# Performance work log

Hardware: AMD Instinct MI355X
Metric: run time of the kernel (lower is better)

## Reference

```python
import jax, jax.numpy as jnp
import numpy as np

N = 100000   # nodes
E = 1200000  # edges
B = 64       # graphs
IN_DIM, HID, OUT_DIM = 128, 64, 2
N_HIDDEN = 2  # num_layers - 1 hidden GCN layers
EPS = 1e-5


def setup_inputs() -> dict:
    key = jax.random.key(0)
    ks = jax.random.split(key, 12)
    x = jax.random.normal(ks[0], (N, IN_DIM), dtype=jnp.float32)
    edge_index = jax.random.randint(ks[1], (2, E), 0, N, dtype=jnp.int64)
    batch = jnp.sort(jax.random.randint(ks[2], (N,), 0, B, dtype=jnp.int64))
    # Glorot-ish init for GCN linear weights (stored as [in, out])
    W_in = jax.random.normal(ks[3], (IN_DIM, HID), dtype=jnp.float32) / np.sqrt(IN_DIM)
    b_in = jnp.zeros((HID,), dtype=jnp.float32)
    W_h = jax.random.normal(ks[4], (N_HIDDEN, HID, HID), dtype=jnp.float32) / np.sqrt(HID)
    b_h = jnp.zeros((N_HIDDEN, HID), dtype=jnp.float32)
    W_out = jax.random.normal(ks[5], (HID, OUT_DIM), dtype=jnp.float32) / np.sqrt(HID)
    b_out = jnp.zeros((OUT_DIM,), dtype=jnp.float32)
    bn_gamma = jnp.ones((3, HID), dtype=jnp.float32)   # num_layers batch norms
    bn_beta = jnp.zeros((3, HID), dtype=jnp.float32)
    return {"x": x, "W_in": W_in, "b_in": b_in, "W_h": W_h, "b_h": b_h,
            "W_out": W_out, "b_out": b_out, "bn_gamma": bn_gamma,
            "bn_beta": bn_beta, "edge_index": edge_index, "batch": batch}


def _gcn_conv(h, W, b, src, dst, dinv):
    # PyG GCNConv: h' = D^-1/2 (A + I) D^-1/2 (h W) + b
    h = h @ W
    norm = dinv[src] * dinv[dst]                       # [E]
    agg = jax.ops.segment_sum(h[src] * norm[:, None], dst, num_segments=N)
    agg = agg + h * (dinv * dinv)[:, None]             # self-loop term
    return agg + b


def _batchnorm(h, gamma, beta):
    m = h.mean(axis=0)
    v = h.var(axis=0)  # biased, matches torch BN normalization
    return (h - m) * jax.lax.rsqrt(v + EPS) * gamma + beta


def reference(x, W_in, b_in, W_h, b_h, W_out, b_out, bn_gamma, bn_beta, edge_index, batch):
    src, dst = edge_index[0], edge_index[1]
    # degree with self-loops (edge weight 1)
    deg = jax.ops.segment_sum(jnp.ones((E,), x.dtype), dst, num_segments=N) + 1.0
    dinv = deg ** -0.5

    h = jax.nn.relu(_gcn_conv(x, W_in, b_in, src, dst, dinv))
    h = _batchnorm(h, bn_gamma[0], bn_beta[0])
    for i in range(N_HIDDEN):
        res = h
        h = jax.nn.relu(_gcn_conv(h, W_h[i], b_h[i], src, dst, dinv))
        h = _batchnorm(h, bn_gamma[i + 1], bn_beta[i + 1])
        h = h + res  # shapes match (HID == HID)
    h = _gcn_conv(h, W_out, b_out, src, dst, dinv)

    # global mean pool over batch segments
    sums = jax.ops.segment_sum(h, batch, num_segments=B)
    cnt = jax.ops.segment_sum(jnp.ones((N,), h.dtype), batch, num_segments=B)
    return sums / jnp.maximum(cnt, 1.0)[:, None]
```

## Files before the change

### kernel.cpp

```cpp
#include <hip/hip_runtime.h>
#include <hip/hip_fp16.h>


#define NN 100000
#define NE 1200000
#define NBATCH 64
#define IND 128
#define HID 64
#define EPSF 1e-5f
#define NBUCK 782
#define NPB 128
#define BCAP 2048

__global__ void k_escatter(const int* __restrict__ src, const int* __restrict__ dst,
                           int* __restrict__ bcur, unsigned long long* __restrict__ ebuf) {
  __shared__ int lh[NBUCK];
  __shared__ int lbase[NBUCK];
  int tid = threadIdx.x;
  for (int i = tid; i < NBUCK; i += 256) lh[i] = 0;
  __syncthreads();
  int base4 = blockIdx.x * 1024;
  int sv[16], dv[16], rk[16];
#pragma unroll
  for (int j = 0; j < 4; j++) {
    int i4 = base4 + j * 256 + tid;
    if (i4 * 4 < NE) {
      int4 s4 = ((const int4*)src)[i4];
      int4 d4 = ((const int4*)dst)[i4];
      sv[4 * j + 0] = s4.x; dv[4 * j + 0] = d4.x;
      sv[4 * j + 1] = s4.y; dv[4 * j + 1] = d4.y;
      sv[4 * j + 2] = s4.z; dv[4 * j + 2] = d4.z;
      sv[4 * j + 3] = s4.w; dv[4 * j + 3] = d4.w;
      rk[4 * j + 0] = atomicAdd(&lh[d4.x >> 7], 1);
      rk[4 * j + 1] = atomicAdd(&lh[d4.y >> 7], 1);
      rk[4 * j + 2] = atomicAdd(&lh[d4.z >> 7], 1);
      rk[4 * j + 3] = atomicAdd(&lh[d4.w >> 7], 1);
    } else {
      dv[4 * j + 0] = -1; dv[4 * j + 1] = -1;
      dv[4 * j + 2] = -1; dv[4 * j + 3] = -1;
    }
  }
  __syncthreads();
  for (int i = tid; i < NBUCK; i += 256) {
    int v = lh[i];
    lbase[i] = v ? atomicAdd(&bcur[i], v) : 0;
  }
  __syncthreads();
#pragma unroll
  for (int j = 0; j < 16; j++) {
    if (dv[j] >= 0) {
      int b = dv[j] >> 7;
      ebuf[(size_t)b * BCAP + lbase[b] + rk[j]] =
          (unsigned long long)(unsigned)sv[j] | ((unsigned long long)(unsigned)dv[j] << 32);
    }
  }
}

__global__ void k_bucket_csr(const unsigned long long* __restrict__ ebuf,
                             const int* __restrict__ bcur, int2* __restrict__ rc,
                             int* __restrict__ col) {
  __shared__ int ldeg[NPB];
  __shared__ int lcur[NPB];
  __shared__ int sred[NPB];
  int b = blockIdx.x, tid = threadIdx.x;
  int nbase = b * NPB;
  int e0 = b * BCAP;
  int cnt = bcur[b];
  if (tid < NPB) ldeg[tid] = 0;
  __syncthreads();
  for (int e = tid; e < cnt; e += 256) {
    int d = (int)(ebuf[e0 + e] >> 32) - nbase;
    atomicAdd(&ldeg[d], 1);
  }
  __syncthreads();
  if (tid < NPB) sred[tid] = ldeg[tid];
  __syncthreads();
  for (int off = 1; off < NPB; off <<= 1) {
    int v = 0;
    if (tid < NPB && tid >= off) v = sred[tid - off];
    __syncthreads();
    if (tid < NPB) sred[tid] += v;
    __syncthreads();
  }
  if (tid < NPB) {
    int excl = sred[tid] - ldeg[tid];
    lcur[tid] = excl;
    int gn = nbase + tid;
    if (gn < NN) rc[gn] = make_int2(e0 + excl, ldeg[tid]);
  }
  __syncthreads();
  for (int e = tid; e < cnt; e += 256) {
    unsigned long long p = ebuf[e0 + e];
    int s = (int)(unsigned)p;
    int d = (int)(p >> 32) - nbase;
    int r = atomicAdd(&lcur[d], 1);
    col[e0 + r] = s;
  }
}

__global__ __launch_bounds__(512) void k_mmA(const float* __restrict__ X,
                                             const float* __restrict__ W,
                                             const int2* __restrict__ rc,
                                             __half* __restrict__ T, int nrows) {
  __shared__ float xs[64 * 65];
  int tid = threadIdx.x;
  int rbase = blockIdx.x * 64;
  int q8 = __builtin_amdgcn_readfirstlane(tid >> 6);
  int r = tid & 63;
  int r65 = r * 65;
  float4 acc[2];
  acc[0] = {0.f, 0.f, 0.f, 0.f};
  acc[1] = {0.f, 0.f, 0.f, 0.f};

  for (int ch = 0; ch < 2; ch++) {
#pragma unroll
    for (int i = 0; i < 2; i++) {
      int f = i * 512 + tid;
      int rr = f >> 4, kq = f & 15;
      int gr = rbase + rr;
      int grc = gr < nrows ? gr : nrows - 1;
      float4 v = *(const float4*)(X + (size_t)grc * 128 + ch * 64 + 4 * kq);
      float* p = xs + rr * 65 + 4 * kq;
      p[0] = v.x; p[1] = v.y; p[2] = v.z; p[3] = v.w;
    }
    __syncthreads();
    const float* Wb = W + ch * 64 * 64 + q8 * 8;
#pragma unroll 4
    for (int k = 0; k < 64; k++) {
      float xk = xs[r65 + k];
      const float4* wr = (const float4*)(Wb + (size_t)k * 64);
      float4 w0 = wr[0], w1 = wr[1];
      acc[0].x = fmaf(xk, w0.x, acc[0].x);
      acc[0].y = fmaf(xk, w0.y, acc[0].y);
      acc[0].z = fmaf(xk, w0.z, acc[0].z);
      acc[0].w = fmaf(xk, w0.w, acc[0].w);
      acc[1].x = fmaf(xk, w1.x, acc[1].x);
      acc[1].y = fmaf(xk, w1.y, acc[1].y);
      acc[1].z = fmaf(xk, w1.z, acc[1].z);
      acc[1].w = fmaf(xk, w1.w, acc[1].w);
    }
    if (ch == 0) __syncthreads();
  }

  int row = rbase + r;
  if (row < nrows) {
    float dv = rsqrtf((float)rc[row].y + 1.0f);
    __half2 o2[4];
    o2[0] = __floats2half2_rn(acc[0].x * dv, acc[0].y * dv);
    o2[1] = __floats2half2_rn(acc[0].z * dv, acc[0].w * dv);
    o2[2] = __floats2half2_rn(acc[1].x * dv, acc[1].y * dv);
    o2[3] = __floats2half2_rn(acc[1].z * dv, acc[1].w * dv);
    *(float4*)(T + (size_t)row * 64 + q8 * 8) = *(float4*)&o2[0];
  }
}

__global__ __launch_bounds__(512) void k_mmB(const __half* __restrict__ G,
                                             const double* __restrict__ st,
                                             const float* __restrict__ gamma,
                                             const float* __restrict__ beta,
                                             const float* __restrict__ res,
                                             float* __restrict__ Hside,
                                             const float* __restrict__ W,
                                             const int2* __restrict__ rc,
                                             __half* __restrict__ T, int nrows) {
  __shared__ float xs[64 * 65];
  __shared__ float scl[128];
  int tid = threadIdx.x;
  if (tid < 64) {
    double m = st[tid] / (double)NN;
    double var = st[64 + tid] / (double)NN - m * m;
    float scale = gamma[tid] * rsqrtf((float)var + EPSF);
    scl[tid] = scale;
    scl[64 + tid] = beta[tid] - (float)m * scale;
  }
  __syncthreads();

  int rbase = blockIdx.x * 64;
  {
    int rr = tid >> 3;
    int kc = tid & 7;
    int gr = rbase + rr;
    int grc = gr < nrows ? gr : nrows - 1;
    int fb = kc * 8;
    float4 raw = *(const float4*)(G + (size_t)grc * 64 + fb);
    const __half2* hp = (const __half2*)&raw;
    float v[8];
    float2 t0 = __half22float2(hp[0]); v[0] = t0.x; v[1] = t0.y;
    float2 t1 = __half22float2(hp[1]); v[2] = t1.x; v[3] = t1.y;
    float2 t2 = __half22float2(hp[2]); v[4] = t2.x; v[5] = t2.y;
    float2 t3 = __half22float2(hp[3]); v[6] = t3.x; v[7] = t3.y;
#pragma unroll
    for (int j = 0; j < 8; j++) v[j] = v[j] * scl[fb + j] + scl[64 + fb + j];
    if (res != nullptr) {
      float4 r0 = *(const float4*)(res + (size_t)grc * 64 + fb);
      float4 r1 = *(const float4*)(res + (size_t)grc * 64 + fb + 4);
      v[0] += r0.x; v[1] += r0.y; v[2] += r0.z; v[3] += r0.w;
      v[4] += r1.x; v[5] += r1.y; v[6] += r1.z; v[7] += r1.w;
    }
    if (gr < nrows) {
      *(float4*)(Hside + (size_t)gr * 64 + fb) = make_float4(v[0], v[1], v[2], v[3]);
      *(float4*)(Hside + (size_t)gr * 64 + fb + 4) = make_float4(v[4], v[5], v[6], v[7]);
    }
    float* p = xs + rr * 65 + fb;
#pragma unroll
    for (int j = 0; j < 8; j++) p[j] = v[j];
  }
  __syncthreads();

  int q8 = __builtin_amdgcn_readfirstlane(tid >> 6);
  int r = tid & 63;
  int r65 = r * 65;
  float4 acc[2];
  acc[0] = {0.f, 0.f, 0.f, 0.f};
  acc[1] = {0.f, 0.f, 0.f, 0.f};
  const float* Wb = W + q8 * 8;
#pragma unroll 4
  for (int k = 0; k < 64; k++) {
    float xk = xs[r65 + k];
    const float4* wr = (const float4*)(Wb + (size_t)k * 64);
    float4 w0 = wr[0], w1 = wr[1];
    acc[0].x = fmaf(xk, w0.x, acc[0].x);
    acc[0].y = fmaf(xk, w0.y, acc[0].y);
    acc[0].z = fmaf(xk, w0.z, acc[0].z);
    acc[0].w = fmaf(xk, w0.w, acc[0].w);
    acc[1].x = fmaf(xk, w1.x, acc[1].x);
    acc[1].y = fmaf(xk, w1.y, acc[1].y);
    acc[1].z = fmaf(xk, w1.z, acc[1].z);
    acc[1].w = fmaf(xk, w1.w, acc[1].w);
  }

  int row = rbase + r;
  if (row < nrows) {
    float dv = rsqrtf((float)rc[row].y + 1.0f);
    __half2 o2[4];
    o2[0] = __floats2half2_rn(acc[0].x * dv, acc[0].y * dv);
    o2[1] = __floats2half2_rn(acc[0].z * dv, acc[0].w * dv);
    o2[2] = __floats2half2_rn(acc[1].x * dv, acc[1].y * dv);
    o2[3] = __floats2half2_rn(acc[1].z * dv, acc[1].w * dv);
    *(float4*)(T + (size_t)row * 64 + q8 * 8) = *(float4*)&o2[0];
  }
}

__global__ void k_agg64(const __half* __restrict__ T, const int2* __restrict__ rc,
                        const int* __restrict__ col, const float* __restrict__ bias,
                        __half* __restrict__ G, int relu) {
  int lane = threadIdx.x & 63;
  int wv = threadIdx.x >> 6;
  int node = blockIdx.x * 4 + wv;
  if (node >= NN) return;
  int grp = lane >> 4;
  int q = lane & 15;
  int2 sc = rc[node];
  int s = sc.x;
  int c = sc.y;
  float di = rsqrtf((float)c + 1.0f);
  float2 rs = *(const float2*)(T + (size_t)node * 64 + q * 4);
  float4 acc = {0.f, 0.f, 0.f, 0.f};
  for (int i = 0; i < c; i += 16) {
    int j0 = i + grp, j1 = j0 + 4, j2 = j0 + 8, j3 = j0 + 12;
    int s0 = col[s + (j0 < c ? j0 : 0)];
    int s1 = col[s + (j1 < c ? j1 : 0)];
    int s2 = col[s + (j2 < c ? j2 : 0)];
    int s3 = col[s + (j3 < c ? j3 : 0)];
    float2 r0 = *(const float2*)(T + (size_t)s0 * 64 + q * 4);
    float2 r1 = *(const float2*)(T + (size_t)s1 * 64 + q * 4);
    float2 r2 = *(const float2*)(T + (size_t)s2 * 64 + q * 4);
    float2 r3 = *(const float2*)(T + (size_t)s3 * 64 + q * 4);
    float w0 = j0 < c ? 1.f : 0.f;
    float w1 = j1 < c ? 1.f : 0.f;
    float w2 = j2 < c ? 1.f : 0.f;
    float w3 = j3 < c ? 1.f : 0.f;
    {
      __half2* p = (__half2*)&r0;
      float2 lo = __half22float2(p[0]), hi = __half22float2(p[1]);
      acc.x = fmaf(w0, lo.x, acc.x); acc.y = fmaf(w0, lo.y, acc.y);
      acc.z = fmaf(w0, hi.x, acc.z); acc.w = fmaf(w0, hi.y, acc.w);
    }
    {
      __half2* p = (__half2*)&r1;
      float2 lo = __half22float2(p[0]), hi = __half22float2(p[1]);
      acc.x = fmaf(w1, lo.x, acc.x); acc.y = fmaf(w1, lo.y, acc.y);
      acc.z = fmaf(w1, hi.x, acc.z); acc.w = fmaf(w1, hi.y, acc.w);
    }
    {
      __half2* p = (__half2*)&r2;
      float2 lo = __half22float2(p[0]), hi = __half22float2(p[1]);
      acc.x = fmaf(w2, lo.x, acc.x); acc.y = fmaf(w2, lo.y, acc.y);
      acc.z = fmaf(w2, hi.x, acc.z); acc.w = fmaf(w2, hi.y, acc.w);
    }
    {
      __half2* p = (__half2*)&r3;
      float2 lo = __half22float2(p[0]), hi = __half22float2(p[1]);
      acc.x = fmaf(w3, lo.x, acc.x); acc.y = fmaf(w3, lo.y, acc.y);
      acc.z = fmaf(w3, hi.x, acc.z); acc.w = fmaf(w3, hi.y, acc.w);
    }
  }
  acc.x += __shfl_xor(acc.x, 16, 64);
  acc.y += __shfl_xor(acc.y, 16, 64);
  acc.z += __shfl_xor(acc.z, 16, 64);
  acc.w += __shfl_xor(acc.w, 16, 64);
  acc.x += __shfl_xor(acc.x, 32, 64);
  acc.y += __shfl_xor(acc.y, 32, 64);
  acc.z += __shfl_xor(acc.z, 32, 64);
  acc.w += __shfl_xor(acc.w, 32, 64);
  if (grp == 0) {
    __half2* p = (__half2*)&rs;
    float2 lo = __half22float2(p[0]), hi = __half22float2(p[1]);
    float4 bs = ((const float4*)bias)[q];
    float4 o;
    o.x = (acc.x + lo.x) * di + bs.x;
    o.y = (acc.y + lo.y) * di + bs.y;
    o.z = (acc.z + hi.x) * di + bs.z;
    o.w = (acc.w + hi.y) * di + bs.w;
    if (relu) {
      o.x = fmaxf(o.x, 0.f);
      o.y = fmaxf(o.y, 0.f);
      o.z = fmaxf(o.z, 0.f);
      o.w = fmaxf(o.w, 0.f);
    }
    float2 pk;
    ((__half2*)&pk)[0] = __floats2half2_rn(o.x, o.y);
    ((__half2*)&pk)[1] = __floats2half2_rn(o.z, o.w);
    *(float2*)(G + (size_t)node * 64 + q * 4) = pk;
  }
}

__global__ __launch_bounds__(256) void k_stats(const __half* __restrict__ H,
                                               double* __restrict__ st) {
  int q = threadIdx.x & 15;
  int rg = threadIdx.x >> 4;
  float4 s1 = {0.f, 0.f, 0.f, 0.f};
  float4 s2 = {0.f, 0.f, 0.f, 0.f};
  for (int r = blockIdx.x * 16 + rg; r < NN; r += gridDim.x * 16) {
    float2 raw = *(const float2*)(H + (size_t)r * 64 + q * 4);
    const __half2* hp = (const __half2*)&raw;
    float2 lo = __half22float2(hp[0]), hi = __half22float2(hp[1]);
    s1.x += lo.x; s1.y += lo.y; s1.z += hi.x; s1.w += hi.y;
    s2.x = fmaf(lo.x, lo.x, s2.x); s2.y = fmaf(lo.y, lo.y, s2.y);
    s2.z = fmaf(hi.x, hi.x, s2.z); s2.w = fmaf(hi.y, hi.y, s2.w);
  }
  __shared__ float a[16][16][8];
  a[rg][q][0] = s1.x; a[rg][q][1] = s1.y; a[rg][q][2] = s1.z; a[rg][q][3] = s1.w;
  a[rg][q][4] = s2.x; a[rg][q][5] = s2.y; a[rg][q][6] = s2.z; a[rg][q][7] = s2.w;
  __syncthreads();
  int tid = threadIdx.x;
  if (tid < 128) {
    int f = tid & 63;
    int which = tid >> 6;
    int qq = f >> 2, jj = (f & 3) + which * 4;
    float t = 0.f;
#pragma unroll
    for (int g = 0; g < 16; g++) t += a[g][qq][jj];
    unsafeAtomicAdd(&st[which * 64 + f], (double)t);
  }
}

__global__ void k_bnmmout(const __half* __restrict__ G, const double* __restrict__ st,
                          const float* __restrict__ gamma, const float* __restrict__ beta,
                          const float* __restrict__ res, const float* __restrict__ W,
                          const int2* __restrict__ rc, float* __restrict__ T2,
                          int nrows) {
  __shared__ float Wl[128];
  __shared__ float scl[128];
  int tid = threadIdx.x;
  if (tid < 32) ((float4*)Wl)[tid] = ((const float4*)W)[tid];
  else if (tid >= 64 && tid < 128) {
    int f = tid - 64;
    double m = st[f] / (double)NN;
    double var = st[64 + f] / (double)NN - m * m;
    float scale = gamma[f] * rsqrtf((float)var + EPSF);
    scl[f] = scale;
    scl[64 + f] = beta[f] - (float)m * scale;
  }
  __syncthreads();
  int row = blockIdx.x * 256 + tid;
  if (row >= nrows) return;
  const __half* g = G + (size_t)row * 64;
  const float4* r4 = (const float4*)(res + (size_t)row * 64);
  float a0 = 0.f, a1 = 0.f;
#pragma unroll
  for (int q = 0; q < 16; q++) {
    float2 raw = *(const float2*)(g + q * 4);
    const __half2* hp = (const __half2*)&raw;
    float2 lo = __half22float2(hp[0]), hi = __half22float2(hp[1]);
    float4 rr = r4[q];
    float4 s = ((const float4*)scl)[q];
    float4 sh = ((const float4*)(scl + 64))[q];
    float h0 = lo.x * s.x + sh.x + rr.x;
    float h1 = lo.y * s.y + sh.y + rr.y;
    float h2 = hi.x * s.z + sh.z + rr.z;
    float h3 = hi.y * s.w + sh.w + rr.w;
    const float* wk = Wl + q * 8;
    a0 = fmaf(h0, wk[0], a0); a1 = fmaf(h0, wk[1], a1);
    a0 = fmaf(h1, wk[2], a0); a1 = fmaf(h1, wk[3], a1);
    a0 = fmaf(h2, wk[4], a0); a1 = fmaf(h2, wk[5], a1);
    a0 = fmaf(h3, wk[6], a0); a1 = fmaf(h3, wk[7], a1);
  }
  float dv = rsqrtf((float)rc[row].y + 1.0f);
  T2[(size_t)row * 2 + 0] = a0 * dv;
  T2[(size_t)row * 2 + 1] = a1 * dv;
}

__global__ void k_agg2pool(const float* __restrict__ T2, const int2* __restrict__ rc,
                           const int* __restrict__ col, const float* __restrict__ bias,
                           const int* __restrict__ batch, float* __restrict__ pool,
                           int* __restrict__ pcnt, int* __restrict__ tick,
                           float* __restrict__ out, int nblk) {
  __shared__ float pl[128];
  __shared__ int pc[64];
  __shared__ int lastflag;
  int tid = threadIdx.x;
  if (tid < 128) pl[tid] = 0.f;
  if (tid < 64) pc[tid] = 0;
  __syncthreads();
  int node = blockIdx.x * 256 + tid;
  if (node < NN) {
    int2 sc = rc[node];
    int s = sc.x;
    int c = sc.y;
    float a0 = 0.f, a1 = 0.f;
    for (int i = 0; i < c; i += 4) {
      int j0 = i, j1 = i + 1, j2 = i + 2, j3 = i + 3;
      int s0 = col[s + j0];
      int sA = col[s + (j1 < c ? j1 : j0)];
      int sB = col[s + (j2 < c ? j2 : j0)];
      int sC = col[s + (j3 < c ? j3 : j0)];
      float2 t0 = *(const float2*)(T2 + 2 * (size_t)s0);
      float2 t1 = *(const float2*)(T2 + 2 * (size_t)sA);
      float2 t2 = *(const float2*)(T2 + 2 * (size_t)sB);
      float2 t3 = *(const float2*)(T2 + 2 * (size_t)sC);
      float w1 = j1 < c ? 1.f : 0.f;
      float w2 = j2 < c ? 1.f : 0.f;
      float w3 = j3 < c ? 1.f : 0.f;
      a0 += t0.x; a1 += t0.y;
      a0 = fmaf(w1, t1.x, a0); a1 = fmaf(w1, t1.y, a1);
      a0 = fmaf(w2, t2.x, a0); a1 = fmaf(w2, t2.y, a1);
      a0 = fmaf(w3, t3.x, a0); a1 = fmaf(w3, t3.y, a1);
    }
    float di = rsqrtf((float)c + 1.0f);
    float2 tn = *(const float2*)(T2 + 2 * (size_t)node);
    float v0 = (a0 + tn.x) * di + bias[0];
    float v1 = (a1 + tn.y) * di + bias[1];
    int bb = batch[node];
    atomicAdd(&pl[bb * 2 + 0], v0);
    atomicAdd(&pl[bb * 2 + 1], v1);
    atomicAdd(&pc[bb], 1);
  }
  __syncthreads();
  if (tid < 128 && pl[tid] != 0.f) unsafeAtomicAdd(&pool[tid], pl[tid]);
  if (tid < 64 && pc[tid] != 0) atomicAdd(&pcnt[tid], pc[tid]);
  __syncthreads();
  if (tid == 0) {
    __threadfence();
    int old = atomicAdd(tick, 1);
    lastflag = (old == nblk - 1) ? 1 : 0;
  }
  __syncthreads();
  if (lastflag && tid < 128) {
    float v = unsafeAtomicAdd(&pool[tid], 0.f);
    int c = atomicAdd(&pcnt[tid >> 1], 0);
    out[tid] = v / (float)(c > 0 ? c : 1);
  }
}

extern "C" void kernel_launch(void* const* d_in, const int* in_sizes, int n_in,
                              void* d_out, int out_size, void* d_ws, size_t ws_size,
                              hipStream_t stream) {
  (void)in_sizes; (void)n_in; (void)out_size; (void)ws_size;
  const float* x     = (const float*)d_in[0];
  const float* W_in  = (const float*)d_in[1];
  const float* b_in  = (const float*)d_in[2];
  const float* W_h   = (const float*)d_in[3];
  const float* b_h   = (const float*)d_in[4];
  const float* W_out = (const float*)d_in[5];
  const float* b_out = (const float*)d_in[6];
  const float* gamma = (const float*)d_in[7];
  const float* beta  = (const float*)d_in[8];
  const int*   ei    = (const int*)d_in[9];
  const int*   batch = (const int*)d_in[10];
  const int* src = ei;
  const int* dst = ei + NE;
  float* out = (float*)d_out;

  char* w = (char*)d_ws;
  size_t off = 0;
  auto alloc = [&](size_t bytes) -> void* {
    void* p = (void*)(w + off);
    off += (bytes + 511) & ~(size_t)511;
    return p;
  };
  int2*   rc    = (int2*)alloc((size_t)NN * 8);
  int*    col   = (int*)alloc((size_t)NBUCK * BCAP * 4);
  char*   zzone = (char*)alloc(7680);
  double* stats = (double*)zzone;
  float*  pool  = (float*)(zzone + 3072);
  int*    pcnt  = (int*)(zzone + 3584);
  int*    tick  = (int*)(zzone + 3840);
  int*    bcur  = (int*)(zzone + 4096);
  __half* Ga    = (__half*)alloc((size_t)NN * HID * 2);
  __half* Gb    = (__half*)alloc((size_t)NN * HID * 2);
  float*  hA    = (float*)alloc((size_t)NN * HID * 4);
  float*  hB    = (float*)alloc((size_t)NN * HID * 4);
  __half* Th    = (__half*)alloc((size_t)NN * HID * 2);
  float*  T2    = (float*)alloc((size_t)NN * 2 * 4);
  unsigned long long* ebuf = (unsigned long long*)hA;

  hipMemsetAsync(zzone, 0, 7424, stream);

  k_escatter<<<293, 256, 0, stream>>>(src, dst, bcur, ebuf);
  k_bucket_csr<<<NBUCK, 256, 0, stream>>>(ebuf, bcur, rc, col);

  const int mmgrid = (NN + 63) / 64;

  k_mmA<<<mmgrid, 512, 0, stream>>>(x, W_in, rc, Th, NN);
  k_agg64<<<(NN + 3) / 4, 256, 0, stream>>>(Th, rc, col, b_in, Ga, 1);
  k_stats<<<512, 256, 0, stream>>>(Ga, stats);

  k_mmB<<<mmgrid, 512, 0, stream>>>(Ga, stats, gamma, beta, nullptr, hA, W_h,
                                    rc, Th, NN);
  k_agg64<<<(NN + 3) / 4, 256, 0, stream>>>(Th, rc, col, b_h, Gb, 1);
  k_stats<<<512, 256, 0, stream>>>(Gb, stats + 128);

  k_mmB<<<mmgrid, 512, 0, stream>>>(Gb, stats + 128, gamma + 64, beta + 64, hA,
                                    hB, W_h + HID * HID, rc, Th, NN);
  k_agg64<<<(NN + 3) / 4, 256, 0, stream>>>(Th, rc, col, b_h + HID, Ga, 1);
  k_stats<<<512, 256, 0, stream>>>(Ga, stats + 256);

  k_bnmmout<<<(NN + 255) / 256, 256, 0, stream>>>(Ga, stats + 256, gamma + 128,
                                                  beta + 128, hB, W_out, rc, T2, NN);
  const int pgrid = (NN + 255) / 256;
  k_agg2pool<<<pgrid, 256, 0, stream>>>(T2, rc, col, b_out, batch, pool,
                                        pcnt, tick, out, pgrid);
}
```

Measured before the change: 372.6 us.

## Store residual activations in fp16 and widen aggregation gathers to 16-byte loads

The residual/side activation buffers hA and hB go from fp32 to fp16. k_mmB and k_bnmmout now read and write them as packed half vectors, which halves the bytes moved for these full-size node arrays. The aggregation kernel now uses 8 lanes per 64-feature row with 16-byte loads, covering 32 neighbour slots per loop iteration instead of 16. That issues fewer, wider gathers but wastes more lanes on low-degree nodes. The residual path adds one more fp16 rounding per layer, which can cost a little accuracy.

```diff
diff --git a/kernel.cpp b/kernel.cpp
--- a/kernel.cpp
+++ b/kernel.cpp
@@ -158,8 +158,8 @@
                                              const double* __restrict__ st,
                                              const float* __restrict__ gamma,
                                              const float* __restrict__ beta,
-                                             const float* __restrict__ res,
-                                             float* __restrict__ Hside,
+                                             const __half* __restrict__ res,
+                                             __half* __restrict__ Hside,
                                              const float* __restrict__ W,
                                              const int2* __restrict__ rc,
                                              __half* __restrict__ T, int nrows) {
@@ -192,14 +192,20 @@
 #pragma unroll
     for (int j = 0; j < 8; j++) v[j] = v[j] * scl[fb + j] + scl[64 + fb + j];
     if (res != nullptr) {
-      float4 r0 = *(const float4*)(res + (size_t)grc * 64 + fb);
-      float4 r1 = *(const float4*)(res + (size_t)grc * 64 + fb + 4);
-      v[0] += r0.x; v[1] += r0.y; v[2] += r0.z; v[3] += r0.w;
-      v[4] += r1.x; v[5] += r1.y; v[6] += r1.z; v[7] += r1.w;
+      float4 rraw = *(const float4*)(res + (size_t)grc * 64 + fb);
+      const __half2* rp = (const __half2*)&rraw;
+      float2 a0 = __half22float2(rp[0]); v[0] += a0.x; v[1] += a0.y;
+      float2 a1 = __half22float2(rp[1]); v[2] += a1.x; v[3] += a1.y;
+      float2 a2 = __half22float2(rp[2]); v[4] += a2.x; v[5] += a2.y;
+      float2 a3 = __half22float2(rp[3]); v[6] += a3.x; v[7] += a3.y;
     }
     if (gr < nrows) {
-      *(float4*)(Hside + (size_t)gr * 64 + fb) = make_float4(v[0], v[1], v[2], v[3]);
-      *(float4*)(Hside + (size_t)gr * 64 + fb + 4) = make_float4(v[4], v[5], v[6], v[7]);
+      __half2 hpk[4];
+      hpk[0] = __floats2half2_rn(v[0], v[1]);
+      hpk[1] = __floats2half2_rn(v[2], v[3]);
+      hpk[2] = __floats2half2_rn(v[4], v[5]);
+      hpk[3] = __floats2half2_rn(v[6], v[7]);
+      *(float4*)(Hside + (size_t)gr * 64 + fb) = *(float4*)hpk;
     }
     float* p = xs + rr * 65 + fb;
 #pragma unroll
@@ -248,80 +254,90 @@
   int wv = threadIdx.x >> 6;
   int node = blockIdx.x * 4 + wv;
   if (node >= NN) return;
-  int grp = lane >> 4;
-  int q = lane & 15;
+  int grp = lane >> 3;
+  int q = lane & 7;
   int2 sc = rc[node];
   int s = sc.x;
   int c = sc.y;
   float di = rsqrtf((float)c + 1.0f);
-  float2 rs = *(const float2*)(T + (size_t)node * 64 + q * 4);
-  float4 acc = {0.f, 0.f, 0.f, 0.f};
-  for (int i = 0; i < c; i += 16) {
-    int j0 = i + grp, j1 = j0 + 4, j2 = j0 + 8, j3 = j0 + 12;
+  float4 rs = *(const float4*)(T + (size_t)node * 64 + q * 8);
+  float acc[8] = {0.f, 0.f, 0.f, 0.f, 0.f, 0.f, 0.f, 0.f};
+  for (int i = 0; i < c; i += 32) {
+    int j0 = i + grp, j1 = j0 + 8, j2 = j0 + 16, j3 = j0 + 24;
     int s0 = col[s + (j0 < c ? j0 : 0)];
     int s1 = col[s + (j1 < c ? j1 : 0)];
     int s2 = col[s + (j2 < c ? j2 : 0)];
     int s3 = col[s + (j3 < c ? j3 : 0)];
-    float2 r0 = *(const float2*)(T + (size_t)s0 * 64 + q * 4);
-    float2 r1 = *(const float2*)(T + (size_t)s1 * 64 + q * 4);
-    float2 r2 = *(const float2*)(T + (size_t)s2 * 64 + q * 4);
-    float2 r3 = *(const float2*)(T + (size_t)s3 * 64 + q * 4);
+    float4 r0 = *(const float4*)(T + (size_t)s0 * 64 + q * 8);
+    float4 r1 = *(const float4*)(T + (size_t)s1 * 64 + q * 8);
+    float4 r2 = *(const float4*)(T + (size_t)s2 * 64 + q * 8);
+    float4 r3 = *(const float4*)(T + (size_t)s3 * 64 + q * 8);
     float w0 = j0 < c ? 1.f : 0.f;
     float w1 = j1 < c ? 1.f : 0.f;
     float w2 = j2 < c ? 1.f : 0.f;
     float w3 = j3 < c ? 1.f : 0.f;
     {
-      __half2* p = (__half2*)&r0;
-      float2 lo = __half22float2(p[0]), hi = __half22float2(p[1]);
-      acc.x = fmaf(w0, lo.x, acc.x); acc.y = fmaf(w0, lo.y, acc.y);
-      acc.z = fmaf(w0, hi.x, acc.z); acc.w = fmaf(w0, hi.y, acc.w);
+      const __half2* p = (const __half2*)&r0;
+      float2 f0 = __half22float2(p[0]), f1 = __half22float2(p[1]);
+      float2 f2 = __half22float2(p[2]), f3 = __half22float2(p[3]);
+      acc[0] = fmaf(w0, f0.x, acc[0]); acc[1] = fmaf(w0, f0.y, acc[1]);
+      acc[2] = fmaf(w0, f1.x, acc[2]); acc[3] = fmaf(w0, f1.y, acc[3]);
+      acc[4] = fmaf(w0, f2.x, acc[4]); acc[5] = fmaf(w0, f2.y, acc[5]);
+      acc[6] = fmaf(w0, f3.x, acc[6]); acc[7] = fmaf(w0, f3.y, acc[7]);
     }
     {
-      __half2* p = (__half2*)&r1;
-      float2 lo = __half22float2(p[0]), hi = __half22float2(p[1]);
-      acc.x = fmaf(w1, lo.x, acc.x); acc.y = fmaf(w1, lo.y, acc.y);
-      acc.z = fmaf(w1, hi.x, acc.z); acc.w = fmaf(w1, hi.y, acc.w);
+      const __half2* p = (const __half2*)&r1;
+      float2 f0 = __half22float2(p[0]), f1 = __half22float2(p[1]);
+      float2 f2 = __half22float2(p[2]), f3 = __half22float2(p[3]);
+      acc[0] = fmaf(w1, f0.x, acc[0]); acc[1] = fmaf(w1, f0.y, acc[1]);
+      acc[2] = fmaf(w1, f1.x, acc[2]); acc[3] = fmaf(w1, f1.y, acc[3]);
+      acc[4] = fmaf(w1, f2.x, acc[4]); acc[5] = fmaf(w1, f2.y, acc[5]);
+      acc[6] = fmaf(w1, f3.x, acc[6]); acc[7] = fmaf(w1, f3.y, acc[7]);
     }
     {
-      __half2* p = (__half2*)&r2;
-      float2 lo = __half22float2(p[0]), hi = __half22float2(p[1]);
-      acc.x = fmaf(w2, lo.x, acc.x); acc.y = fmaf(w2, lo.y, acc.y);
-      acc.z = fmaf(w2, hi.x, acc.z); acc.w = fmaf(w2, hi.y, acc.w);
+      const __half2* p = (const __half2*)&r2;
+      float2 f0 = __half22float2(p[0]), f1 = __half22float2(p[1]);
+      float2 f2 = __half22float2(p[2]), f3 = __half22float2(p[3]);
+      acc[0] = fmaf(w2, f0.x, acc[0]); acc[1] = fmaf(w2, f0.y, acc[1]);
+      acc[2] = fmaf(w2, f1.x, acc[2]); acc[3] = fmaf(w2, f1.y, acc[3]);
+      acc[4] = fmaf(w2, f2.x, acc[4]); acc[5] = fmaf(w2, f2.y, acc[5]);
+      acc[6] = fmaf(w2, f3.x, acc[6]); acc[7] = fmaf(w2, f3.y, acc[7]);
     }
     {
-      __half2* p = (__half2*)&r3;
-      float2 lo = __half22float2(p[0]), hi = __half22float2(p[1]);
-      acc.x = fmaf(w3, lo.x, acc.x); acc.y = fmaf(w3, lo.y, acc.y);
-      acc.z = fmaf(w3, hi.x, acc.z); acc.w = fmaf(w3, hi.y, acc.w);
-    }
-  }
-  acc.x += __shfl_xor(acc.x, 16, 64);
-  acc.y += __shfl_xor(acc.y, 16, 64);
-  acc.z += __shfl_xor(acc.z, 16, 64);
-  acc.w += __shfl_xor(acc.w, 16, 64);
-  acc.x += __shfl_xor(acc.x, 32, 64);
-  acc.y += __shfl_xor(acc.y, 32, 64);
-  acc.z += __shfl_xor(acc.z, 32, 64);
-  acc.w += __shfl_xor(acc.w, 32, 64);
+      const __half2* p = (const __half2*)&r3;
+      float2 f0 = __half22float2(p[0]), f1 = __half22float2(p[1]);
+      float2 f2 = __half22float2(p[2]), f3 = __half22float2(p[3]);
+      acc[0] = fmaf(w3, f0.x, acc[0]); acc[1] = fmaf(w3, f0.y, acc[1]);
+      acc[2] = fmaf(w3, f1.x, acc[2]); acc[3] = fmaf(w3, f1.y, acc[3]);
+      acc[4] = fmaf(w3, f2.x, acc[4]); acc[5] = fmaf(w3, f2.y, acc[5]);
+      acc[6] = fmaf(w3, f3.x, acc[6]); acc[7] = fmaf(w3, f3.y, acc[7]);
+    }
+  }
+#pragma unroll
+  for (int off = 8; off < 64; off <<= 1) {
+#pragma unroll
+    for (int j = 0; j < 8; j++) acc[j] += __shfl_xor(acc[j], off, 64);
+  }
   if (grp == 0) {
-    __half2* p = (__half2*)&rs;
-    float2 lo = __half22float2(p[0]), hi = __half22float2(p[1]);
-    float4 bs = ((const float4*)bias)[q];
-    float4 o;
-    o.x = (acc.x + lo.x) * di + bs.x;
-    o.y = (acc.y + lo.y) * di + bs.y;
-    o.z = (acc.z + hi.x) * di + bs.z;
-    o.w = (acc.w + hi.y) * di + bs.w;
-    if (relu) {
-      o.x = fmaxf(o.x, 0.f);
-      o.y = fmaxf(o.y, 0.f);
-      o.z = fmaxf(o.z, 0.f);
-      o.w = fmaxf(o.w, 0.f);
-    }
-    float2 pk;
-    ((__half2*)&pk)[0] = __floats2half2_rn(o.x, o.y);
-    ((__half2*)&pk)[1] = __floats2half2_rn(o.z, o.w);
-    *(float2*)(G + (size_t)node * 64 + q * 4) = pk;
+    const __half2* p = (const __half2*)&rs;
+    float2 f0 = __half22float2(p[0]), f1 = __half22float2(p[1]);
+    float2 f2 = __half22float2(p[2]), f3 = __half22float2(p[3]);
+    float sv[8] = {f0.x, f0.y, f1.x, f1.y, f2.x, f2.y, f3.x, f3.y};
+    float4 b0 = ((const float4*)bias)[q * 2];
+    float4 b1 = ((const float4*)bias)[q * 2 + 1];
+    float bb[8] = {b0.x, b0.y, b0.z, b0.w, b1.x, b1.y, b1.z, b1.w};
+    float o[8];
+#pragma unroll
+    for (int j = 0; j < 8; j++) {
+      o[j] = (acc[j] + sv[j]) * di + bb[j];
+      if (relu) o[j] = fmaxf(o[j], 0.f);
+    }
+    __half2 pk[4];
+    pk[0] = __floats2half2_rn(o[0], o[1]);
+    pk[1] = __floats2half2_rn(o[2], o[3]);
+    pk[2] = __floats2half2_rn(o[4], o[5]);
+    pk[3] = __floats2half2_rn(o[6], o[7]);
+    *(float4*)(G + (size_t)node * 64 + q * 8) = *(float4*)pk;
   }
 }
 
@@ -357,7 +373,7 @@
 
 __global__ void k_bnmmout(const __half* __restrict__ G, const double* __restrict__ st,
                           const float* __restrict__ gamma, const float* __restrict__ beta,
-                          const float* __restrict__ res, const float* __restrict__ W,
+                          const __half* __restrict__ res, const float* __restrict__ W,
                           const int2* __restrict__ rc, float* __restrict__ T2,
                           int nrows) {
   __shared__ float Wl[128];
@@ -376,25 +392,30 @@
   int row = blockIdx.x * 256 + tid;
   if (row >= nrows) return;
   const __half* g = G + (size_t)row * 64;
-  const float4* r4 = (const float4*)(res + (size_t)row * 64);
+  const __half* rr = res + (size_t)row * 64;
   float a0 = 0.f, a1 = 0.f;
 #pragma unroll
-  for (int q = 0; q < 16; q++) {
-    float2 raw = *(const float2*)(g + q * 4);
-    const __half2* hp = (const __half2*)&raw;
-    float2 lo = __half22float2(hp[0]), hi = __half22float2(hp[1]);
-    float4 rr = r4[q];
-    float4 s = ((const float4*)scl)[q];
-    float4 sh = ((const float4*)(scl + 64))[q];
-    float h0 = lo.x * s.x + sh.x + rr.x;
-    float h1 = lo.y * s.y + sh.y + rr.y;
-    float h2 = hi.x * s.z + sh.z + rr.z;
-    float h3 = hi.y * s.w + sh.w + rr.w;
-    const float* wk = Wl + q * 8;
-    a0 = fmaf(h0, wk[0], a0); a1 = fmaf(h0, wk[1], a1);
-    a0 = fmaf(h1, wk[2], a0); a1 = fmaf(h1, wk[3], a1);
-    a0 = fmaf(h2, wk[4], a0); a1 = fmaf(h2, wk[5], a1);
-    a0 = fmaf(h3, wk[6], a0); a1 = fmaf(h3, wk[7], a1);
+  for (int qq = 0; qq < 8; qq++) {
+    int fb = qq * 8;
+    float4 graw = *(const float4*)(g + fb);
+    float4 rraw = *(const float4*)(rr + fb);
+    const __half2* gp = (const __half2*)&graw;
+    const __half2* rp = (const __half2*)&rraw;
+    float gv[8], rv[8];
+    float2 t0 = __half22float2(gp[0]); gv[0] = t0.x; gv[1] = t0.y;
+    float2 t1 = __half22float2(gp[1]); gv[2] = t1.x; gv[3] = t1.y;
+    float2 t2 = __half22float2(gp[2]); gv[4] = t2.x; gv[5] = t2.y;
+    float2 t3 = __half22float2(gp[3]); gv[6] = t3.x; gv[7] = t3.y;
+    float2 u0 = __half22float2(rp[0]); rv[0] = u0.x; rv[1] = u0.y;
+    float2 u1 = __half22float2(rp[1]); rv[2] = u1.x; rv[3] = u1.y;
+    float2 u2 = __half22float2(rp[2]); rv[4] = u2.x; rv[5] = u2.y;
+    float2 u3 = __half22float2(rp[3]); rv[6] = u3.x; rv[7] = u3.y;
+#pragma unroll
+    for (int j = 0; j < 8; j++) {
+      float h = gv[j] * scl[fb + j] + scl[64 + fb + j] + rv[j];
+      a0 = fmaf(h, Wl[(fb + j) * 2 + 0], a0);
+      a1 = fmaf(h, Wl[(fb + j) * 2 + 1], a1);
+    }
   }
   float dv = rsqrtf((float)rc[row].y + 1.0f);
   T2[(size_t)row * 2 + 0] = a0 * dv;
@@ -499,8 +520,8 @@
   int*    bcur  = (int*)(zzone + 4096);
   __half* Ga    = (__half*)alloc((size_t)NN * HID * 2);
   __half* Gb    = (__half*)alloc((size_t)NN * HID * 2);
-  float*  hA    = (float*)alloc((size_t)NN * HID * 4);
-  float*  hB    = (float*)alloc((size_t)NN * HID * 4);
+  __half* hA    = (__half*)alloc((size_t)NN * HID * 2);
+  __half* hB    = (__half*)alloc((size_t)NN * HID * 2);
   __half* Th    = (__half*)alloc((size_t)NN * HID * 2);
   float*  T2    = (float*)alloc((size_t)NN * 2 * 4);
   unsigned long long* ebuf = (unsigned long long*)hA;
```

New measurement: 369.1 us. About the same (-0.9%).
